# Kernel optimization log

Measured on AMD Instinct MI355X. Metric: run time of the kernel, lower is better.

## Reference

```python
import jax, jax.numpy as jnp
import numpy as np

SAMPLE_RATE = 22050
N_FILTER_BANKS = 64
HOP_LENGTH = 512
BATCH = 4
N_FRAMES = 500
N_SAMPLES = N_FRAMES * HOP_LENGTH


def _frame_mean_weights(n_frames, n_samples):
    """Per-frame weights w s.t. mean over time of linear(align_corners=True)
    upsampling of a length-n_frames signal equals w @ signal (exact same math,
    since the interpolation is linear in the frame values)."""
    pos = jnp.linspace(0.0, n_frames - 1.0, n_samples)
    lo = jnp.clip(jnp.floor(pos).astype(jnp.int32), 0, n_frames - 2)
    frac = pos - lo
    w = jnp.zeros(n_frames, dtype=jnp.float32)
    w = w.at[lo].add(1.0 - frac).at[lo + 1].add(frac)
    return w / n_samples


def setup_inputs() -> dict:
    key = jax.random.key(0)
    k1, k2 = jax.random.split(key)
    filter_magnitudes = jax.random.uniform(k1, (BATCH, N_FRAMES, N_FILTER_BANKS), dtype=jnp.float32)
    noise = jax.random.normal(k2, (BATCH, N_SAMPLES), dtype=jnp.float32)
    return {"filter_magnitudes": filter_magnitudes, "noise": noise}


def reference(filter_magnitudes, noise):
    B, n_frames, n_banks = filter_magnitudes.shape
    n_samples = noise.shape[1]

    noise_fft = jnp.fft.rfft(noise, axis=1)                      # (B, n_freq) complex
    freqs = jnp.fft.rfftfreq(n_samples, 1.0 / SAMPLE_RATE)       # (n_freq,)
    filter_freqs = jnp.logspace(np.log10(20.0), np.log10(SAMPLE_RATE / 2.0), n_banks).astype(jnp.float32)

    # mean over time of the linearly-upsampled magnitudes (exact, no big buffer)
    mean_w = _frame_mean_weights(n_frames, n_samples)            # (n_frames,)
    mean_mag = jnp.einsum('bfk,f->bk', filter_magnitudes, mean_w)  # (B, n_banks)

    # vectorized log-distance filterbank weights: (n_freq, n_banks)
    D = jnp.log(freqs + 1e-7)[:, None] - jnp.log(filter_freqs + 1e-7)[None, :]
    W = jnp.exp(-(D ** 2) / 0.5)
    W = W / (W.sum(axis=1, keepdims=True) + 1e-7)

    filter_response = mean_mag @ W.T                              # (B, n_freq)
    filtered_fft = noise_fft * filter_response
    return jnp.fft.irfft(filtered_fft, n=n_samples, axis=1)      # (B, n_samples)
```

## Files before the change

### kernel.cpp

```cpp
#include <hip/hip_runtime.h>
#include <math.h>

#define NS 256000
#define N1 512
#define N2 500
#define PI_F 3.14159265358979323846f

typedef float2 cplx;

__device__ __forceinline__ cplx cadd(cplx a, cplx b){ return make_float2(a.x+b.x, a.y+b.y); }
__device__ __forceinline__ cplx csub(cplx a, cplx b){ return make_float2(a.x-b.x, a.y-b.y); }
__device__ __forceinline__ cplx cmul(cplx a, cplx b){ return make_float2(a.x*b.x-a.y*b.y, a.x*b.y+a.y*b.x); }
__device__ __forceinline__ cplx cmulc(cplx a, cplx b){ return make_float2(a.x*b.x+a.y*b.y, a.y*b.x-a.x*b.y); }
__device__ __forceinline__ cplx crotf(cplx v, float ang){
    float sn = __sinf(ang), cs = __cosf(ang);
    return make_float2(v.x*cs - v.y*sn, v.x*sn + v.y*cs);
}
__device__ __forceinline__ int PX(int e){ return e + (e>>4); }
__device__ __forceinline__ int rev8_3(int k){ return ((k&7)<<6) | (k&0x38) | (k>>6); }

#define U1PAD 545
#define U2PAD 537
#define WFENCE() asm volatile("s_waitcnt lgkmcnt(0)" ::: "memory")
#define LDS_BARRIER() do{ asm volatile("s_waitcnt lgkmcnt(0)" ::: "memory"); __builtin_amdgcn_s_barrier(); }while(0)

template<bool INV>
__device__ __forceinline__ void dft4(const cplx* a, cplx* b){
    cplx t0=cadd(a[0],a[2]), t1=csub(a[0],a[2]), t2=cadd(a[1],a[3]), t3=csub(a[1],a[3]);
    b[0]=cadd(t0,t2); b[2]=csub(t0,t2);
    if(!INV){ b[1]=make_float2(t1.x+t3.y, t1.y-t3.x); b[3]=make_float2(t1.x-t3.y, t1.y+t3.x); }
    else    { b[1]=make_float2(t1.x-t3.y, t1.y+t3.x); b[3]=make_float2(t1.x+t3.y, t1.y-t3.x); }
}

template<bool INV>
__device__ __forceinline__ void dft8(const cplx* a, cplx* b){
    cplx ev[4]={a[0],a[2],a[4],a[6]}, od[4]={a[1],a[3],a[5],a[7]};
    cplx C[4], D[4];
    dft4<INV>(ev, C); dft4<INV>(od, D);
    const float s = 0.70710678118654752f;
    const float sg = INV ? 1.f : -1.f;
    cplx d1 = cmul(D[1], make_float2( s, sg*s));
    cplx d2 = cmul(D[2], make_float2(0.f, sg ));
    cplx d3 = cmul(D[3], make_float2(-s, sg*s));
    b[0]=cadd(C[0],D[0]); b[4]=csub(C[0],D[0]);
    b[1]=cadd(C[1],d1);   b[5]=csub(C[1],d1);
    b[2]=cadd(C[2],d2);   b[6]=csub(C[2],d2);
    b[3]=cadd(C[3],d3);   b[7]=csub(C[3],d3);
}

template<bool INV>
__device__ __forceinline__ void dft5(const cplx* a, cplx* b){
    const float c1=0.30901699437494742f, s1=0.95105651629515357f;
    const float c2=-0.80901699437494745f, s2=0.58778525229247312f;
    const float sg = INV ? 1.f : -1.f;
    cplx W[5];
    W[0]=make_float2(1.f,0.f);
    W[1]=make_float2(c1, sg*s1); W[2]=make_float2(c2, sg*s2);
    W[3]=make_float2(c2,-sg*s2); W[4]=make_float2(c1,-sg*s1);
#pragma unroll
    for(int u=0;u<5;++u){
        cplx acc = a[0];
        int idx = 0;
#pragma unroll
        for(int r=1;r<5;++r){
            idx += u; if(idx >= 5) idx -= 5;
            acc = cadd(acc, cmul(a[r], W[idx]));
        }
        b[u] = acc;
    }
}

template<int R, int L, int TMUL, bool INV, int NN>
__device__ __forceinline__ void wstage(cplx* Uw, const cplx* tab, int lane){
    constexpr int m = L / R;
    constexpr int nb = NN / R;
    constexpr int NIT = (nb + 63) / 64;
    cplx a[NIT][R];
    cplx wt[NIT][R];
    int  bs[NIT];
#pragma unroll
    for(int it=0; it<NIT; ++it){
        int beta = lane + it*64;
        int blk = beta / m;
        int j = beta - blk*m;
        bs[it] = blk*L + j;
        if(beta < nb){
#pragma unroll
            for(int t=0;t<R;++t) a[it][t] = Uw[PX(bs[it] + m*t)];
#pragma unroll
            for(int t=1;t<R;++t) wt[it][t] = tab[TMUL*j*t];
        }
    }
#pragma unroll
    for(int it=0; it<NIT; ++it){
        int beta = lane + it*64;
        if(beta < nb){
            if(INV){
#pragma unroll
                for(int t=1;t<R;++t) a[it][t] = cmulc(a[it][t], wt[it][t]);
            }
            cplx bb[R];
            if constexpr (R==4) dft4<INV>(a[it], bb);
            else if constexpr (R==5) dft5<INV>(a[it], bb);
            else dft8<INV>(a[it], bb);
            if(!INV){
#pragma unroll
                for(int t=1;t<R;++t) bb[t] = cmul(bb[t], wt[it][t]);
            }
#pragma unroll
            for(int t=0;t<R;++t) Uw[PX(bs[it] + m*t)] = bb[t];
        }
    }
}

template<int NTAB, int NTHR>
__device__ __forceinline__ void build_tab(cplx* tab, int tid){
    const float step = -2.f*PI_F/(float)NTAB;
    for(int i = tid; i < NTAB; i += NTHR){
        float a = step*(float)i;
        tab[i] = make_float2(__cosf(a), __sinf(a));
    }
}

__device__ __forceinline__ int p2k2(int p){
    int t1 = p/100; int r = p - 100*t1;
    int t2 = r/20;  r -= 20*t2;
    int t3 = r>>2;  int t4 = r & 3;
    return t1 + 5*t2 + 25*t3 + 125*t4;
}
__device__ __forceinline__ int k22p(int k){
    int t1 = k % 5; int k5 = k/5;
    int t2 = k5 % 5; int k25 = k5/5;
    int t3 = k25 % 5; int t4 = k25/5;
    return 100*t1 + 20*t2 + 4*t3 + t4;
}
__device__ __forceinline__ int colord(int q){
    int j = q>>1, w = q&1;
    if(j == 0) return w ? 256 : 0;
    return w ? 512 - j : j;
}
__device__ __forceinline__ int xcd_chunk(int bid, int n){
    int q = n>>3, r = n&7;
    int x = bid&7, idx = bid>>3;
    return (x < r ? x*(q+1) : r*(q+1) + (x-r)*q) + idx;
}

__device__ __forceinline__ void hpair(cplx Z1, cplx Z2, float ha, float hb,
                                      cplx* zk, cplx* znk){
    float xr = 0.5f*(Z1.x + Z2.x), xi = 0.5f*(Z1.y - Z2.y);
    float yr = 0.5f*(Z1.y + Z2.y), yi = -0.5f*(Z1.x - Z2.x);
    *zk  = make_float2(ha*xr - hb*yi, ha*xi + hb*yr);
    *znk = make_float2(ha*xr + hb*yi, hb*yr - ha*xi);
}

__global__ void __launch_bounds__(256) kFused1(const float* __restrict__ fm,
                                               const float* __restrict__ noise,
                                               float* __restrict__ mmL,
                                               cplx* __restrict__ Y){
    __shared__ float Aarr[500];
    __shared__ float wfr[500];
    __shared__ float part[256];
    __shared__ cplx tab[512];
    __shared__ cplx U[4][U1PAD];
    const int bid = blockIdx.x, tid = threadIdx.x;
    if(bid < 4){
        const int b = bid;
        for(int f = tid; f < 500; f += 256){
            long long i0 = ((long long)f*255999LL + 498LL)/499LL;
            long long i1 = ((long long)(f+1)*255999LL + 498LL)/499LL;
            long long cnt = i1 - i0;
            long long sumi = (i0 + i1 - 1)*cnt/2;
            long long num = 499LL*sumi - cnt*(long long)f*255999LL;
            Aarr[f] = (float)((double)num / 255999.0);
        }
        __syncthreads();
        for(int f = tid; f < 500; f += 256){
            long long i0 = ((long long)f*255999LL + 498LL)/499LL;
            long long i1 = ((long long)(f+1)*255999LL + 498LL)/499LL;
            double w;
            if(f < 499) w = (double)(i1 - i0) - (double)Aarr[f] + (f > 0 ? (double)Aarr[f-1] : 0.0);
            else        w = (double)Aarr[498] + 1.0;
            wfr[f] = (float)(w / (double)NS);
        }
        __syncthreads();
        const int k = tid & 63, seg = tid >> 6;
        float acc = 0.f;
        for(int f = seg*125; f < seg*125 + 125; ++f)
            acc += wfr[f] * fm[(b*500 + f)*64 + k];
        part[seg*64 + k] = acc;
        __syncthreads();
        if(tid < 64) mmL[b*64 + tid] = part[tid] + part[64+tid] + part[128+tid] + part[192+tid];
        return;
    }
    if(bid == 4){
        if(tid < 64){
            double a = log10(20.0), b2 = log10(11025.0);
            double e = a + (b2 - a)*(double)tid/63.0;
            float ff = (float)pow(10.0, e);
            mmL[256 + tid] = logf(ff + 1e-7f);
        }
        return;
    }
    const int g = xcd_chunk(bid - 5, 250);
    const int s = g / 125;
    const int n2base = (g - s*125) * 4;
    const int lane = tid & 63, w = tid >> 6;
    build_tab<512,256>(tab, tid);
    const float* xa = noise + (size_t)(2*s)*NS + n2base;
    const float* xb = noise + (size_t)(2*s+1)*NS + n2base;
#pragma unroll
    for(int k=0;k<8;++k){
        int i = tid + 256*k;
        int n1 = i >> 2, ws = i & 3;
        U[ws][PX(n1)] = make_float2(xa[n1*500 + ws], xb[n1*500 + ws]);
    }
    __syncthreads();
    cplx* Uw = U[w];
    wstage<8,512, 1,false,512>(Uw, tab, lane); WFENCE();
    wstage<8, 64, 8,false,512>(Uw, tab, lane); WFENCE();
    wstage<8,  8,64,false,512>(Uw, tab, lane); WFENCE();
    const int n2 = n2base + w;
    cplx* yp = Y + ((size_t)s*500 + n2)*N1;
    const float tw = -2.f*PI_F/(float)NS;
#pragma unroll
    for(int t=0;t<8;++t){
        int q = lane + 64*t;
        int c = colord(q);
        cplx v = Uw[PX(rev8_3(c))];
        v = crotf(v, tw*(float)(n2*c));
        yp[q] = v;
    }
}

__global__ void __launch_bounds__(256) kFused2(cplx* __restrict__ Y,
                                               const float* __restrict__ mmL){
    __shared__ cplx tab[500];
    __shared__ cplx U[4][U2PAD];
    __shared__ float Hr[2][2][500];
    __shared__ float HrX[2][500];
    __shared__ float mmS[2][64];
    __shared__ float lgf[64];
    const int tid = threadIdx.x, lane = tid & 63, w = tid >> 6;
    const int L = xcd_chunk(blockIdx.x, 256);
    const int su = L >> 7;
    const int j0 = 2*(L & 127);
    const int s0 = 2*j0;
    cplx* Ybase = Y + (size_t)su*500*512 + s0;
    cplx rg[8];
#pragma unroll
    for(int k=0;k<8;++k){
        int e = tid + 256*k;
        rg[k] = (e < 2000) ? Ybase[(e>>2)*512 + (e&3)] : make_float2(0.f,0.f);
    }
    build_tab<500,256>(tab, tid);
    if(tid < 128) mmS[tid>>6][tid&63] = mmL[2*su*64 + tid];
    if(tid < 64)  lgf[tid] = mmL[256 + tid];
    LDS_BARRIER();
    const int special = (j0 == 0);
    const int nrows = special ? 3 : 2;
    const float invN = 1.f/(float)NS;
    for(int idx = tid; idx < nrows*500; idx += 256){
        int r = idx / 500;
        int p = idx - 500*r;
        int k1 = (r==0) ? j0 : ((r==1) ? j0+1 : 256);
        int k2 = p2k2(p);
        int kf = k1 + 512*k2;
        int kk = min(kf, NS - kf);
        float lf = logf((float)kk*(22050.f/(float)NS) + 1e-7f);
        float wsum = 0.f, a0 = 0.f, a1 = 0.f;
#pragma unroll
        for(int jb=0;jb<64;++jb){
            float d = lf - lgf[jb];
            float e2 = __expf(-2.f*d*d);
            wsum += e2; a0 += e2*mmS[0][jb]; a1 += e2*mmS[1][jb];
        }
        float inv = invN/(wsum + 1e-7f);
        if(r < 2){ Hr[r][0][p] = a0*inv; Hr[r][1][p] = a1*inv; }
        else     { HrX[0][p]   = a0*inv; HrX[1][p]   = a1*inv; }
    }
#pragma unroll
    for(int k=0;k<8;++k){
        int e = tid + 256*k;
        if(e < 2000) U[e&3][PX(e>>2)] = rg[k];
    }
    __syncthreads();
    cplx* Uw = U[w];
    wstage<5,500,  1,false,500>(Uw, tab, lane); WFENCE();
    wstage<5,100,  5,false,500>(Uw, tab, lane); WFENCE();
    wstage<5, 20, 25,false,500>(Uw, tab, lane); WFENCE();
    wstage<4,  4,125,false,500>(Uw, tab, lane);
    __syncthreads();
    {
        const int u = w >> 1, cw = w & 1;
        cplx* UA = U[2*u];
        cplx* UB = U[2*u + 1];
        if(special && u == 0){
            if(cw == 0){
#pragma unroll 1
                for(int t=0;t<8;++t){
                    int p = lane + 64*t;
                    if(p < 500){
                        int k2 = p2k2(p);
                        int pp = k22p((500 - k2) % 500);
                        if(p <= pp){
                            cplx Z1 = UA[PX(p)], Z2 = UA[PX(pp)];
                            cplx zk, znk;
                            hpair(Z1, Z2, Hr[0][0][p], Hr[0][1][p], &zk, &znk);
                            UA[PX(p)]  = zk;
                            UA[PX(pp)] = znk;
                        }
                    }
                }
            } else {
#pragma unroll 1
                for(int t=0;t<4;++t){
                    int p = lane + 64*t;
                    if(p < 250){
                        cplx Z1 = UB[PX(p)], Z2 = UB[PX(499-p)];
                        cplx zk, znk;
                        hpair(Z1, Z2, HrX[0][p], HrX[1][p], &zk, &znk);
                        UB[PX(p)]     = zk;
                        UB[PX(499-p)] = znk;
                    }
                }
            }
        } else {
            const float* H0 = Hr[u][0];
            const float* H1 = Hr[u][1];
#pragma unroll 1
            for(int t=0;t<4;++t){
                int pl = lane + 64*t;
                if(pl < 250){
                    int p = cw*250 + pl;
                    cplx Z1 = UA[PX(p)], Z2 = UB[PX(499-p)];
                    cplx zk, znk;
                    hpair(Z1, Z2, H0[p], H1[p], &zk, &znk);
                    UA[PX(p)]     = zk;
                    UB[PX(499-p)] = znk;
                }
            }
        }
    }
    __syncthreads();
    wstage<4,  4,125,true,500>(Uw, tab, lane); WFENCE();
    wstage<5, 20, 25,true,500>(Uw, tab, lane); WFENCE();
    wstage<5,100,  5,true,500>(Uw, tab, lane); WFENCE();
    wstage<5,500,  1,true,500>(Uw, tab, lane);
    __syncthreads();
    const float tw2 = 2.f*PI_F/(float)NS;
#pragma unroll
    for(int k=0;k<8;++k){
        int e = tid + 256*k;
        if(e < 2000){
            int n2 = e >> 2, sl = e & 3;
            int cc = colord(s0 + sl);
            cplx v = U[sl][PX(n2)];
            v = crotf(v, tw2*(float)(n2*cc));
            Ybase[n2*512 + sl] = v;
        }
    }
}

__global__ void __launch_bounds__(256) kFused3(const cplx* __restrict__ Y,
                                               float* __restrict__ out){
    __shared__ cplx tab[512];
    __shared__ cplx U[4][U1PAD];
    const int tid = threadIdx.x, lane = tid & 63, w = tid >> 6;
    const int g = xcd_chunk(blockIdx.x, 250);
    const int s = g / 125;
    const int n2base = (g - s*125) * 4;
    build_tab<512,256>(tab, tid);
    const cplx* yp = Y + ((size_t)s*500 + n2base)*N1;
#pragma unroll
    for(int k=0;k<8;++k){
        int i = tid + 256*k;
        int ws = i >> 9, q = i & 511;
        cplx v = yp[(size_t)ws*N1 + q];
        U[ws][PX(rev8_3(colord(q)))] = v;
    }
    __syncthreads();
    cplx* Uw = U[w];
    wstage<8,  8,64,true,512>(Uw, tab, lane); WFENCE();
    wstage<8, 64, 8,true,512>(Uw, tab, lane); WFENCE();
    wstage<8,512, 1,true,512>(Uw, tab, lane);
    __syncthreads();
    float* oa = out + (size_t)(2*s)*NS + n2base;
    float* ob = out + (size_t)(2*s+1)*NS + n2base;
#pragma unroll
    for(int k=0;k<8;++k){
        int i = tid + 256*k;
        int n1 = i >> 2, ws = i & 3;
        cplx v = U[ws][PX(n1)];
        oa[n1*500 + ws] = v.x;
        ob[n1*500 + ws] = v.y;
    }
}

extern "C" void kernel_launch(void* const* d_in, const int* in_sizes, int n_in,
                              void* d_out, int out_size, void* d_ws, size_t ws_size,
                              hipStream_t stream) {
    const float* fm = (const float*)d_in[0];
    const float* noise = (const float*)d_in[1];
    float* out = (float*)d_out;

    char* ws = (char*)d_ws;
    cplx*  Y   = (cplx*)ws;
    float* mmL = (float*)(ws + 4194304);

    kFused1<<<255, 256, 0, stream>>>(fm, noise, mmL, Y);
    kFused2<<<256, 256, 0, stream>>>(Y, mmL);
    kFused3<<<250, 256, 0, stream>>>(Y, out);
}
```

Before: 90.59 us.

## Merge three FFT kernels into one phase-switched kernel with noinline stage functions

Replaces the three separate kernels with a single kernel selected by a phase argument, using one dynamic shared-memory buffer carved by offsets. The templated FFT stage code is replaced by __noinline__ radix-8/5/4 stage functions with shift or reciprocal-multiply index math, presumably to shrink code size and register pressure. It also swaps the double-precision pow/log for fast float exp/log in the filter-frequency setup. The risks are call overhead from the noinline functions and slightly different precision in the log-frequency values.

```diff
diff --git a/kernel.cpp b/kernel.cpp
--- a/kernel.cpp
+++ b/kernel.cpp
@@ -19,8 +19,11 @@
 __device__ __forceinline__ int PX(int e){ return e + (e>>4); }
 __device__ __forceinline__ int rev8_3(int k){ return ((k&7)<<6) | (k&0x38) | (k>>6); }
 
-#define U1PAD 545
-#define U2PAD 537
+#define UPAD 545
+#define U_OFF   4096u
+#define EX_OFF  21536u
+#define SMEM_BYTES 34816
+
 #define WFENCE() asm volatile("s_waitcnt lgkmcnt(0)" ::: "memory")
 #define LDS_BARRIER() do{ asm volatile("s_waitcnt lgkmcnt(0)" ::: "memory"); __builtin_amdgcn_s_barrier(); }while(0)
 
@@ -70,55 +73,84 @@
     }
 }
 
-template<int R, int L, int TMUL, bool INV, int NN>
-__device__ __forceinline__ void wstage(cplx* Uw, const cplx* tab, int lane){
-    constexpr int m = L / R;
-    constexpr int nb = NN / R;
-    constexpr int NIT = (nb + 63) / 64;
-    cplx a[NIT][R];
-    cplx wt[NIT][R];
-    int  bs[NIT];
-#pragma unroll
-    for(int it=0; it<NIT; ++it){
-        int beta = lane + it*64;
-        int blk = beta / m;
-        int j = beta - blk*m;
-        bs[it] = blk*L + j;
-        if(beta < nb){
-#pragma unroll
-            for(int t=0;t<R;++t) a[it][t] = Uw[PX(bs[it] + m*t)];
-#pragma unroll
-            for(int t=1;t<R;++t) wt[it][t] = tab[TMUL*j*t];
-        }
-    }
-#pragma unroll
-    for(int it=0; it<NIT; ++it){
-        int beta = lane + it*64;
-        if(beta < nb){
+template<bool INV>
+__device__ __noinline__ void stage8(unsigned uoff, int lane, int sh){
+    extern __shared__ char smem[];
+    cplx* tab = (cplx*)smem;
+    cplx* Uw  = (cplx*)(smem + uoff);
+    const int m = 1 << sh;
+    const int blk = lane >> sh, j = lane & (m-1);
+    const int base = (blk << (sh+3)) + j;
+    const int ts = 6 - sh;
+    cplx a[8], wt[8];
+#pragma unroll
+    for(int t=0;t<8;++t) a[t] = Uw[PX(base + (t<<sh))];
+#pragma unroll
+    for(int t=1;t<8;++t) wt[t] = tab[(j*t) << ts];
+    if(INV){
+#pragma unroll
+        for(int t=1;t<8;++t) a[t] = cmulc(a[t], wt[t]);
+    }
+    cplx bb[8];
+    dft8<INV>(a,bb);
+    if(!INV){
+#pragma unroll
+        for(int t=1;t<8;++t) bb[t] = cmul(bb[t], wt[t]);
+    }
+#pragma unroll
+    for(int t=0;t<8;++t) Uw[PX(base + (t<<sh))] = bb[t];
+}
+
+template<bool INV>
+__device__ __noinline__ void stage5(unsigned uoff, int lane, int m, unsigned recip, int tmul){
+    extern __shared__ char smem[];
+    cplx* tab = (cplx*)smem;
+    cplx* Uw  = (cplx*)(smem + uoff);
+#pragma unroll
+    for(int it=0; it<2; ++it){
+        int beta = lane + 64*it;
+        if(beta < 100){
+            int blk = (int)(((unsigned)beta*recip)>>16);
+            int j = beta - blk*m;
+            int base = blk*(5*m) + j;
+            cplx a[5], wt[5];
+#pragma unroll
+            for(int t=0;t<5;++t) a[t] = Uw[PX(base + m*t)];
+#pragma unroll
+            for(int t=1;t<5;++t) wt[t] = tab[tmul*j*t];
             if(INV){
 #pragma unroll
-                for(int t=1;t<R;++t) a[it][t] = cmulc(a[it][t], wt[it][t]);
-            }
-            cplx bb[R];
-            if constexpr (R==4) dft4<INV>(a[it], bb);
-            else if constexpr (R==5) dft5<INV>(a[it], bb);
-            else dft8<INV>(a[it], bb);
+                for(int t=1;t<5;++t) a[t] = cmulc(a[t], wt[t]);
+            }
+            cplx bb[5];
+            dft5<INV>(a,bb);
             if(!INV){
 #pragma unroll
-                for(int t=1;t<R;++t) bb[t] = cmul(bb[t], wt[it][t]);
-            }
-#pragma unroll
-            for(int t=0;t<R;++t) Uw[PX(bs[it] + m*t)] = bb[t];
-        }
-    }
-}
-
-template<int NTAB, int NTHR>
-__device__ __forceinline__ void build_tab(cplx* tab, int tid){
-    const float step = -2.f*PI_F/(float)NTAB;
-    for(int i = tid; i < NTAB; i += NTHR){
-        float a = step*(float)i;
-        tab[i] = make_float2(__cosf(a), __sinf(a));
+                for(int t=1;t<5;++t) bb[t] = cmul(bb[t], wt[t]);
+            }
+#pragma unroll
+            for(int t=0;t<5;++t) Uw[PX(base + m*t)] = bb[t];
+        }
+    }
+}
+
+template<bool INV>
+__device__ __noinline__ void stage4(unsigned uoff, int lane){
+    extern __shared__ char smem[];
+    cplx* Uw = (cplx*)(smem + uoff);
+#pragma unroll
+    for(int it=0; it<2; ++it){
+        int beta = lane + 64*it;
+        if(beta < 125){
+            int base = beta*4;
+            cplx a[4];
+#pragma unroll
+            for(int t=0;t<4;++t) a[t] = Uw[PX(base+t)];
+            cplx bb[4];
+            dft4<INV>(a,bb);
+#pragma unroll
+            for(int t=0;t<4;++t) Uw[PX(base+t)] = bb[t];
+        }
     }
 }
 
@@ -153,246 +185,251 @@
     *znk = make_float2(ha*xr + hb*yi, hb*yr - ha*xi);
 }
 
-__global__ void __launch_bounds__(256) kFused1(const float* __restrict__ fm,
-                                               const float* __restrict__ noise,
-                                               float* __restrict__ mmL,
-                                               cplx* __restrict__ Y){
-    __shared__ float Aarr[500];
-    __shared__ float wfr[500];
-    __shared__ float part[256];
-    __shared__ cplx tab[512];
-    __shared__ cplx U[4][U1PAD];
+__device__ __forceinline__ void build_tab(cplx* tab, int tid, int ntab){
+    const float step = -2.f*PI_F/(float)ntab;
+    for(int i = tid; i < ntab; i += 256){
+        float a = step*(float)i;
+        tab[i] = make_float2(__cosf(a), __sinf(a));
+    }
+}
+
+__global__ void __launch_bounds__(256) kAll(const float* __restrict__ fm,
+                                            const float* __restrict__ noise,
+                                            float* __restrict__ out,
+                                            cplx* __restrict__ Y,
+                                            float* __restrict__ mmL,
+                                            int phase){
+    extern __shared__ char smem[];
+    cplx* tab = (cplx*)smem;
     const int bid = blockIdx.x, tid = threadIdx.x;
-    if(bid < 4){
-        const int b = bid;
-        for(int f = tid; f < 500; f += 256){
-            long long i0 = ((long long)f*255999LL + 498LL)/499LL;
-            long long i1 = ((long long)(f+1)*255999LL + 498LL)/499LL;
-            long long cnt = i1 - i0;
-            long long sumi = (i0 + i1 - 1)*cnt/2;
-            long long num = 499LL*sumi - cnt*(long long)f*255999LL;
-            Aarr[f] = (float)((double)num / 255999.0);
-        }
-        __syncthreads();
-        for(int f = tid; f < 500; f += 256){
-            long long i0 = ((long long)f*255999LL + 498LL)/499LL;
-            long long i1 = ((long long)(f+1)*255999LL + 498LL)/499LL;
-            double w;
-            if(f < 499) w = (double)(i1 - i0) - (double)Aarr[f] + (f > 0 ? (double)Aarr[f-1] : 0.0);
-            else        w = (double)Aarr[498] + 1.0;
-            wfr[f] = (float)(w / (double)NS);
-        }
-        __syncthreads();
-        const int k = tid & 63, seg = tid >> 6;
-        float acc = 0.f;
-        for(int f = seg*125; f < seg*125 + 125; ++f)
-            acc += wfr[f] * fm[(b*500 + f)*64 + k];
-        part[seg*64 + k] = acc;
-        __syncthreads();
-        if(tid < 64) mmL[b*64 + tid] = part[tid] + part[64+tid] + part[128+tid] + part[192+tid];
+    const int lane = tid & 63, w = tid >> 6;
+    const unsigned uoffw = U_OFF + (unsigned)w*(UPAD*8u);
+    cplx* Ucol0 = (cplx*)(smem + U_OFF);
+
+    if(phase == 0){
+        if(bid < 4){
+            float* Aarr = (float*)(smem + EX_OFF);
+            float* wfr  = (float*)(smem + EX_OFF + 2000);
+            float* part = (float*)(smem + EX_OFF + 4000);
+            const int b = bid;
+            for(int f = tid; f < 500; f += 256){
+                long long i0 = ((long long)f*255999LL + 498LL)/499LL;
+                long long i1 = ((long long)(f+1)*255999LL + 498LL)/499LL;
+                long long cnt = i1 - i0;
+                long long sumi = (i0 + i1 - 1)*cnt/2;
+                long long num = 499LL*sumi - cnt*(long long)f*255999LL;
+                Aarr[f] = (float)((double)num / 255999.0);
+            }
+            __syncthreads();
+            for(int f = tid; f < 500; f += 256){
+                long long i0 = ((long long)f*255999LL + 498LL)/499LL;
+                long long i1 = ((long long)(f+1)*255999LL + 498LL)/499LL;
+                double ww;
+                if(f < 499) ww = (double)(i1 - i0) - (double)Aarr[f] + (f > 0 ? (double)Aarr[f-1] : 0.0);
+                else        ww = (double)Aarr[498] + 1.0;
+                wfr[f] = (float)(ww / (double)NS);
+            }
+            __syncthreads();
+            const int k = tid & 63, seg = tid >> 6;
+            float acc = 0.f;
+            for(int f = seg*125; f < seg*125 + 125; ++f)
+                acc += wfr[f] * fm[(b*500 + f)*64 + k];
+            part[seg*64 + k] = acc;
+            __syncthreads();
+            if(tid < 64) mmL[b*64 + tid] = part[tid] + part[64+tid] + part[128+tid] + part[192+tid];
+            return;
+        }
+        if(bid == 4){
+            if(tid < 64){
+                float ff = __expf(2.99573227f + (float)tid*(6.31218815f/63.f));
+                mmL[256 + tid] = __logf(ff + 1e-7f);
+            }
+            return;
+        }
+        const int g = xcd_chunk(bid - 5, 250);
+        const int s = g / 125;
+        const int n2base = (g - s*125) * 4;
+        build_tab(tab, tid, 512);
+        const float* xa = noise + (size_t)(2*s)*NS + n2base;
+        const float* xb = noise + (size_t)(2*s+1)*NS + n2base;
+#pragma unroll
+        for(int k=0;k<8;++k){
+            int i = tid + 256*k;
+            int n1 = i >> 2, ws = i & 3;
+            (Ucol0 + ws*UPAD)[PX(n1)] = make_float2(xa[n1*500 + ws], xb[n1*500 + ws]);
+        }
+        __syncthreads();
+        stage8<false>(uoffw, lane, 6); WFENCE();
+        stage8<false>(uoffw, lane, 3); WFENCE();
+        stage8<false>(uoffw, lane, 0); WFENCE();
+        const int n2 = n2base + w;
+        cplx* Uw = (cplx*)(smem + uoffw);
+        cplx* yp = Y + ((size_t)s*500 + n2)*N1;
+        const float tw = -2.f*PI_F/(float)NS;
+#pragma unroll
+        for(int t=0;t<8;++t){
+            int q = lane + 64*t;
+            int c = colord(q);
+            cplx v = Uw[PX(rev8_3(c))];
+            v = crotf(v, tw*(float)(n2*c));
+            yp[q] = v;
+        }
         return;
     }
-    if(bid == 4){
-        if(tid < 64){
-            double a = log10(20.0), b2 = log10(11025.0);
-            double e = a + (b2 - a)*(double)tid/63.0;
-            float ff = (float)pow(10.0, e);
-            mmL[256 + tid] = logf(ff + 1e-7f);
-        }
-        return;
-    }
-    const int g = xcd_chunk(bid - 5, 250);
-    const int s = g / 125;
-    const int n2base = (g - s*125) * 4;
-    const int lane = tid & 63, w = tid >> 6;
-    build_tab<512,256>(tab, tid);
-    const float* xa = noise + (size_t)(2*s)*NS + n2base;
-    const float* xb = noise + (size_t)(2*s+1)*NS + n2base;
-#pragma unroll
-    for(int k=0;k<8;++k){
-        int i = tid + 256*k;
-        int n1 = i >> 2, ws = i & 3;
-        U[ws][PX(n1)] = make_float2(xa[n1*500 + ws], xb[n1*500 + ws]);
-    }
-    __syncthreads();
-    cplx* Uw = U[w];
-    wstage<8,512, 1,false,512>(Uw, tab, lane); WFENCE();
-    wstage<8, 64, 8,false,512>(Uw, tab, lane); WFENCE();
-    wstage<8,  8,64,false,512>(Uw, tab, lane); WFENCE();
-    const int n2 = n2base + w;
-    cplx* yp = Y + ((size_t)s*500 + n2)*N1;
-    const float tw = -2.f*PI_F/(float)NS;
-#pragma unroll
-    for(int t=0;t<8;++t){
-        int q = lane + 64*t;
-        int c = colord(q);
-        cplx v = Uw[PX(rev8_3(c))];
-        v = crotf(v, tw*(float)(n2*c));
-        yp[q] = v;
-    }
-}
-
-__global__ void __launch_bounds__(256) kFused2(cplx* __restrict__ Y,
-                                               const float* __restrict__ mmL){
-    __shared__ cplx tab[500];
-    __shared__ cplx U[4][U2PAD];
-    __shared__ float Hr[2][2][500];
-    __shared__ float HrX[2][500];
-    __shared__ float mmS[2][64];
-    __shared__ float lgf[64];
-    const int tid = threadIdx.x, lane = tid & 63, w = tid >> 6;
-    const int L = xcd_chunk(blockIdx.x, 256);
-    const int su = L >> 7;
-    const int j0 = 2*(L & 127);
-    const int s0 = 2*j0;
-    cplx* Ybase = Y + (size_t)su*500*512 + s0;
-    cplx rg[8];
-#pragma unroll
-    for(int k=0;k<8;++k){
-        int e = tid + 256*k;
-        rg[k] = (e < 2000) ? Ybase[(e>>2)*512 + (e&3)] : make_float2(0.f,0.f);
-    }
-    build_tab<500,256>(tab, tid);
-    if(tid < 128) mmS[tid>>6][tid&63] = mmL[2*su*64 + tid];
-    if(tid < 64)  lgf[tid] = mmL[256 + tid];
-    LDS_BARRIER();
-    const int special = (j0 == 0);
-    const int nrows = special ? 3 : 2;
-    const float invN = 1.f/(float)NS;
-    for(int idx = tid; idx < nrows*500; idx += 256){
-        int r = idx / 500;
-        int p = idx - 500*r;
-        int k1 = (r==0) ? j0 : ((r==1) ? j0+1 : 256);
-        int k2 = p2k2(p);
-        int kf = k1 + 512*k2;
-        int kk = min(kf, NS - kf);
-        float lf = logf((float)kk*(22050.f/(float)NS) + 1e-7f);
-        float wsum = 0.f, a0 = 0.f, a1 = 0.f;
-#pragma unroll
-        for(int jb=0;jb<64;++jb){
-            float d = lf - lgf[jb];
-            float e2 = __expf(-2.f*d*d);
-            wsum += e2; a0 += e2*mmS[0][jb]; a1 += e2*mmS[1][jb];
-        }
-        float inv = invN/(wsum + 1e-7f);
-        if(r < 2){ Hr[r][0][p] = a0*inv; Hr[r][1][p] = a1*inv; }
-        else     { HrX[0][p]   = a0*inv; HrX[1][p]   = a1*inv; }
-    }
-#pragma unroll
-    for(int k=0;k<8;++k){
-        int e = tid + 256*k;
-        if(e < 2000) U[e&3][PX(e>>2)] = rg[k];
-    }
-    __syncthreads();
-    cplx* Uw = U[w];
-    wstage<5,500,  1,false,500>(Uw, tab, lane); WFENCE();
-    wstage<5,100,  5,false,500>(Uw, tab, lane); WFENCE();
-    wstage<5, 20, 25,false,500>(Uw, tab, lane); WFENCE();
-    wstage<4,  4,125,false,500>(Uw, tab, lane);
-    __syncthreads();
-    {
-        const int u = w >> 1, cw = w & 1;
-        cplx* UA = U[2*u];
-        cplx* UB = U[2*u + 1];
-        if(special && u == 0){
-            if(cw == 0){
+
+    if(phase == 1){
+        float* HrF = (float*)(smem + EX_OFF);
+        float* HrX = (float*)(smem + EX_OFF + 8000);
+        float* mmS = (float*)(smem + EX_OFF + 12000);
+        float* lgf = (float*)(smem + EX_OFF + 12512);
+        const int L = xcd_chunk(bid, 256);
+        const int su = L >> 7;
+        const int j0 = 2*(L & 127);
+        const int s0 = 2*j0;
+        cplx* Ybase = Y + (size_t)su*500*512 + s0;
+        cplx rg[8];
+#pragma unroll
+        for(int k=0;k<8;++k){
+            int e = tid + 256*k;
+            rg[k] = (e < 2000) ? Ybase[(e>>2)*512 + (e&3)] : make_float2(0.f,0.f);
+        }
+        build_tab(tab, tid, 500);
+        if(tid < 128) mmS[tid] = mmL[2*su*64 + tid];
+        if(tid < 64)  lgf[tid] = mmL[256 + tid];
+        LDS_BARRIER();
+        const int special = (j0 == 0);
+        const int nrows = special ? 3 : 2;
+        const float invN = 1.f/(float)NS;
+        for(int idx = tid; idx < nrows*500; idx += 256){
+            int r = idx / 500;
+            int p = idx - 500*r;
+            int k1 = (r==0) ? j0 : ((r==1) ? j0+1 : 256);
+            int k2 = p2k2(p);
+            int kf = k1 + 512*k2;
+            int kk = min(kf, NS - kf);
+            float lf = __logf((float)kk*(22050.f/(float)NS) + 1e-7f);
+            float wsum = 0.f, a0 = 0.f, a1 = 0.f;
+#pragma unroll 8
+            for(int jb=0;jb<64;++jb){
+                float d = lf - lgf[jb];
+                float e2 = __expf(-2.f*d*d);
+                wsum += e2; a0 += e2*mmS[jb]; a1 += e2*mmS[64+jb];
+            }
+            float inv = invN/(wsum + 1e-7f);
+            if(r < 2){ HrF[(r*2+0)*500 + p] = a0*inv; HrF[(r*2+1)*500 + p] = a1*inv; }
+            else     { HrX[p] = a0*inv; HrX[500+p] = a1*inv; }
+        }
+#pragma unroll
+        for(int k=0;k<8;++k){
+            int e = tid + 256*k;
+            if(e < 2000) (Ucol0 + (e&3)*UPAD)[PX(e>>2)] = rg[k];
+        }
+        __syncthreads();
+        stage5<false>(uoffw, lane, 100,   656u,  1); WFENCE();
+        stage5<false>(uoffw, lane,  20,  3277u,  5); WFENCE();
+        stage5<false>(uoffw, lane,   4, 16384u, 25); WFENCE();
+        stage4<false>(uoffw, lane);
+        __syncthreads();
+        {
+            const int u = w >> 1, cw = w & 1;
+            cplx* UA = Ucol0 + (2*u)*UPAD;
+            cplx* UB = Ucol0 + (2*u+1)*UPAD;
+            if(special && u == 0){
+                if(cw == 0){
 #pragma unroll 1
-                for(int t=0;t<8;++t){
-                    int p = lane + 64*t;
-                    if(p < 500){
-                        int k2 = p2k2(p);
-                        int pp = k22p((500 - k2) % 500);
-                        if(p <= pp){
-                            cplx Z1 = UA[PX(p)], Z2 = UA[PX(pp)];
+                    for(int t=0;t<8;++t){
+                        int p = lane + 64*t;
+                        if(p < 500){
+                            int k2 = p2k2(p);
+                            int pp = k22p((500 - k2) % 500);
+                            if(p <= pp){
+                                cplx Z1 = UA[PX(p)], Z2 = UA[PX(pp)];
+                                cplx zk, znk;
+                                hpair(Z1, Z2, HrF[p], HrF[500+p], &zk, &znk);
+                                UA[PX(p)]  = zk;
+                                UA[PX(pp)] = znk;
+                            }
+                        }
+                    }
+                } else {
+#pragma unroll 1
+                    for(int t=0;t<4;++t){
+                        int p = lane + 64*t;
+                        if(p < 250){
+                            cplx Z1 = UB[PX(p)], Z2 = UB[PX(499-p)];
                             cplx zk, znk;
-                            hpair(Z1, Z2, Hr[0][0][p], Hr[0][1][p], &zk, &znk);
-                            UA[PX(p)]  = zk;
-                            UA[PX(pp)] = znk;
+                            hpair(Z1, Z2, HrX[p], HrX[500+p], &zk, &znk);
+                            UB[PX(p)]     = zk;
+                            UB[PX(499-p)] = znk;
                         }
                     }
                 }
             } else {
+                const float* H0 = HrF + (u*2+0)*500;
+                const float* H1 = HrF + (u*2+1)*500;
 #pragma unroll 1
                 for(int t=0;t<4;++t){
-                    int p = lane + 64*t;
-                    if(p < 250){
-                        cplx Z1 = UB[PX(p)], Z2 = UB[PX(499-p)];
+                    int pl = lane + 64*t;
+                    if(pl < 250){
+                        int p = cw*250 + pl;
+                        cplx Z1 = UA[PX(p)], Z2 = UB[PX(499-p)];
                         cplx zk, znk;
-                        hpair(Z1, Z2, HrX[0][p], HrX[1][p], &zk, &znk);
-                        UB[PX(p)]     = zk;
+                        hpair(Z1, Z2, H0[p], H1[p], &zk, &znk);
+                        UA[PX(p)]     = zk;
                         UB[PX(499-p)] = znk;
                     }
                 }
             }
-        } else {
-            const float* H0 = Hr[u][0];
-            const float* H1 = Hr[u][1];
-#pragma unroll 1
-            for(int t=0;t<4;++t){
-                int pl = lane + 64*t;
-                if(pl < 250){
-                    int p = cw*250 + pl;
-                    cplx Z1 = UA[PX(p)], Z2 = UB[PX(499-p)];
-                    cplx zk, znk;
-                    hpair(Z1, Z2, H0[p], H1[p], &zk, &znk);
-                    UA[PX(p)]     = zk;
-                    UB[PX(499-p)] = znk;
-                }
-            }
-        }
-    }
-    __syncthreads();
-    wstage<4,  4,125,true,500>(Uw, tab, lane); WFENCE();
-    wstage<5, 20, 25,true,500>(Uw, tab, lane); WFENCE();
-    wstage<5,100,  5,true,500>(Uw, tab, lane); WFENCE();
-    wstage<5,500,  1,true,500>(Uw, tab, lane);
-    __syncthreads();
-    const float tw2 = 2.f*PI_F/(float)NS;
-#pragma unroll
-    for(int k=0;k<8;++k){
-        int e = tid + 256*k;
-        if(e < 2000){
-            int n2 = e >> 2, sl = e & 3;
-            int cc = colord(s0 + sl);
-            cplx v = U[sl][PX(n2)];
-            v = crotf(v, tw2*(float)(n2*cc));
-            Ybase[n2*512 + sl] = v;
-        }
-    }
-}
-
-__global__ void __launch_bounds__(256) kFused3(const cplx* __restrict__ Y,
-                                               float* __restrict__ out){
-    __shared__ cplx tab[512];
-    __shared__ cplx U[4][U1PAD];
-    const int tid = threadIdx.x, lane = tid & 63, w = tid >> 6;
-    const int g = xcd_chunk(blockIdx.x, 250);
-    const int s = g / 125;
-    const int n2base = (g - s*125) * 4;
-    build_tab<512,256>(tab, tid);
-    const cplx* yp = Y + ((size_t)s*500 + n2base)*N1;
-#pragma unroll
-    for(int k=0;k<8;++k){
-        int i = tid + 256*k;
-        int ws = i >> 9, q = i & 511;
-        cplx v = yp[(size_t)ws*N1 + q];
-        U[ws][PX(rev8_3(colord(q)))] = v;
-    }
-    __syncthreads();
-    cplx* Uw = U[w];
-    wstage<8,  8,64,true,512>(Uw, tab, lane); WFENCE();
-    wstage<8, 64, 8,true,512>(Uw, tab, lane); WFENCE();
-    wstage<8,512, 1,true,512>(Uw, tab, lane);
-    __syncthreads();
-    float* oa = out + (size_t)(2*s)*NS + n2base;
-    float* ob = out + (size_t)(2*s+1)*NS + n2base;
-#pragma unroll
-    for(int k=0;k<8;++k){
-        int i = tid + 256*k;
-        int n1 = i >> 2, ws = i & 3;
-        cplx v = U[ws][PX(n1)];
-        oa[n1*500 + ws] = v.x;
-        ob[n1*500 + ws] = v.y;
+        }
+        __syncthreads();
+        stage4<true>(uoffw, lane); WFENCE();
+        stage5<true>(uoffw, lane,   4, 16384u, 25); WFENCE();
+        stage5<true>(uoffw, lane,  20,  3277u,  5); WFENCE();
+        stage5<true>(uoffw, lane, 100,   656u,  1);
+        __syncthreads();
+        const float tw2 = 2.f*PI_F/(float)NS;
+#pragma unroll
+        for(int k=0;k<8;++k){
+            int e = tid + 256*k;
+            if(e < 2000){
+                int n2 = e >> 2, sl = e & 3;
+                int cc = colord(s0 + sl);
+                cplx v = (Ucol0 + sl*UPAD)[PX(n2)];
+                v = crotf(v, tw2*(float)(n2*cc));
+                Ybase[n2*512 + sl] = v;
+            }
+        }
+        return;
+    }
+
+    {
+        const int g = xcd_chunk(bid, 250);
+        const int s = g / 125;
+        const int n2base = (g - s*125) * 4;
+        build_tab(tab, tid, 512);
+        const cplx* yp = Y + ((size_t)s*500 + n2base)*N1;
+#pragma unroll
+        for(int k=0;k<8;++k){
+            int i = tid + 256*k;
+            int ws = i >> 9, q = i & 511;
+            cplx v = yp[(size_t)ws*N1 + q];
+            (Ucol0 + ws*UPAD)[PX(rev8_3(colord(q)))] = v;
+        }
+        __syncthreads();
+        stage8<true>(uoffw, lane, 0); WFENCE();
+        stage8<true>(uoffw, lane, 3); WFENCE();
+        stage8<true>(uoffw, lane, 6);
+        __syncthreads();
+        float* oa = out + (size_t)(2*s)*NS + n2base;
+        float* ob = out + (size_t)(2*s+1)*NS + n2base;
+#pragma unroll
+        for(int k=0;k<8;++k){
+            int i = tid + 256*k;
+            int n1 = i >> 2, ws = i & 3;
+            cplx v = (Ucol0 + ws*UPAD)[PX(n1)];
+            oa[n1*500 + ws] = v.x;
+            ob[n1*500 + ws] = v.y;
+        }
     }
 }
 
@@ -407,7 +444,7 @@
     cplx*  Y   = (cplx*)ws;
     float* mmL = (float*)(ws + 4194304);
 
-    kFused1<<<255, 256, 0, stream>>>(fm, noise, mmL, Y);
-    kFused2<<<256, 256, 0, stream>>>(Y, mmL);
-    kFused3<<<250, 256, 0, stream>>>(Y, out);
-}
+    kAll<<<255, 256, SMEM_BYTES, stream>>>(fm, noise, out, Y, mmL, 0);
+    kAll<<<256, 256, SMEM_BYTES, stream>>>(fm, noise, out, Y, mmL, 1);
+    kAll<<<250, 256, SMEM_BYTES, stream>>>(fm, noise, out, Y, mmL, 2);
+}
```

Result: slower. 98.33 us (+8.5%).

## Precompute filter response in first kernel's spare blocks instead of in FFT kernel

Applied to the files above, without the earlier changes.

Moves the per-frequency filterbank response computation (64 exp per bin) out of the second kernel and into 257 extra blocks of the first kernel. Those blocks each recompute the mean magnitudes for all batches and write the response to global memory. The second kernel then only loads the precomputed values alongside its FFT data. This takes the transcendental-heavy work off the critical path of kFused2, at the cost of a larger first launch with redundant mean-magnitude work and extra global traffic.

```diff
diff --git a/kernel.cpp b/kernel.cpp
--- a/kernel.cpp
+++ b/kernel.cpp
@@ -22,7 +22,6 @@
 #define U1PAD 545
 #define U2PAD 537
 #define WFENCE() asm volatile("s_waitcnt lgkmcnt(0)" ::: "memory")
-#define LDS_BARRIER() do{ asm volatile("s_waitcnt lgkmcnt(0)" ::: "memory"); __builtin_amdgcn_s_barrier(); }while(0)
 
 template<bool INV>
 __device__ __forceinline__ void dft4(const cplx* a, cplx* b){
@@ -155,16 +154,18 @@
 
 __global__ void __launch_bounds__(256) kFused1(const float* __restrict__ fm,
                                                const float* __restrict__ noise,
-                                               float* __restrict__ mmL,
+                                               float* __restrict__ HrG,
                                                cplx* __restrict__ Y){
     __shared__ float Aarr[500];
     __shared__ float wfr[500];
     __shared__ float part[256];
+    __shared__ float mmS[4][64];
+    __shared__ float lgf[64];
     __shared__ cplx tab[512];
     __shared__ cplx U[4][U1PAD];
     const int bid = blockIdx.x, tid = threadIdx.x;
-    if(bid < 4){
-        const int b = bid;
+    if(bid >= 250){
+        const int k1 = bid - 250;
         for(int f = tid; f < 500; f += 256){
             long long i0 = ((long long)f*255999LL + 498LL)/499LL;
             long long i1 = ((long long)(f+1)*255999LL + 498LL)/499LL;
@@ -184,24 +185,43 @@
         }
         __syncthreads();
         const int k = tid & 63, seg = tid >> 6;
-        float acc = 0.f;
-        for(int f = seg*125; f < seg*125 + 125; ++f)
-            acc += wfr[f] * fm[(b*500 + f)*64 + k];
-        part[seg*64 + k] = acc;
+#pragma unroll 1
+        for(int b = 0; b < 4; ++b){
+            float acc = 0.f;
+            for(int f = seg*125; f < seg*125 + 125; ++f)
+                acc += wfr[f] * fm[(b*500 + f)*64 + k];
+            part[seg*64 + k] = acc;
+            __syncthreads();
+            if(tid < 64) mmS[b][tid] = part[tid] + part[64+tid] + part[128+tid] + part[192+tid];
+            __syncthreads();
+        }
+        if(tid < 64){
+            float ff = __expf(2.99573227f + (float)tid*(6.31218815f/63.f));
+            lgf[tid] = __logf(ff + 1e-7f);
+        }
         __syncthreads();
-        if(tid < 64) mmL[b*64 + tid] = part[tid] + part[64+tid] + part[128+tid] + part[192+tid];
+        const float invN = 1.f/(float)NS;
+        for(int idx = tid; idx < 1000; idx += 256){
+            int su = (idx >= 500) ? 1 : 0;
+            int p = idx - 500*su;
+            int k2 = p2k2(p);
+            int kf = k1 + 512*k2;
+            int kk = min(kf, NS - kf);
+            float lf = __logf((float)kk*(22050.f/(float)NS) + 1e-7f);
+            float wsum = 0.f, a0 = 0.f, a1 = 0.f;
+#pragma unroll
+            for(int jb=0;jb<64;++jb){
+                float d = lf - lgf[jb];
+                float e2 = __expf(-2.f*d*d);
+                wsum += e2; a0 += e2*mmS[2*su][jb]; a1 += e2*mmS[2*su+1][jb];
+            }
+            float inv = invN/(wsum + 1e-7f);
+            HrG[((size_t)(su*257 + k1)*2 + 0)*500 + p] = a0*inv;
+            HrG[((size_t)(su*257 + k1)*2 + 1)*500 + p] = a1*inv;
+        }
         return;
     }
-    if(bid == 4){
-        if(tid < 64){
-            double a = log10(20.0), b2 = log10(11025.0);
-            double e = a + (b2 - a)*(double)tid/63.0;
-            float ff = (float)pow(10.0, e);
-            mmL[256 + tid] = logf(ff + 1e-7f);
-        }
-        return;
-    }
-    const int g = xcd_chunk(bid - 5, 250);
+    const int g = xcd_chunk(bid, 250);
     const int s = g / 125;
     const int n2base = (g - s*125) * 4;
     const int lane = tid & 63, w = tid >> 6;
@@ -233,18 +253,17 @@
 }
 
 __global__ void __launch_bounds__(256) kFused2(cplx* __restrict__ Y,
-                                               const float* __restrict__ mmL){
+                                               const float* __restrict__ HrG){
     __shared__ cplx tab[500];
     __shared__ cplx U[4][U2PAD];
-    __shared__ float Hr[2][2][500];
+    __shared__ float HrF[2][2][500];
     __shared__ float HrX[2][500];
-    __shared__ float mmS[2][64];
-    __shared__ float lgf[64];
     const int tid = threadIdx.x, lane = tid & 63, w = tid >> 6;
     const int L = xcd_chunk(blockIdx.x, 256);
     const int su = L >> 7;
     const int j0 = 2*(L & 127);
     const int s0 = 2*j0;
+    const int special = (j0 == 0);
     cplx* Ybase = Y + (size_t)su*500*512 + s0;
     cplx rg[8];
 #pragma unroll
@@ -252,31 +271,38 @@
         int e = tid + 256*k;
         rg[k] = (e < 2000) ? Ybase[(e>>2)*512 + (e&3)] : make_float2(0.f,0.f);
     }
+    const float* hsrc = HrG + (size_t)(su*257 + j0)*2*500;
+    float hg[8];
+#pragma unroll
+    for(int k=0;k<8;++k){
+        int e = tid + 256*k;
+        hg[k] = (e < 2000) ? hsrc[e] : 0.f;
+    }
+    float hx[4];
+    if(special){
+        const float* hxsrc = HrG + (size_t)(su*257 + 256)*2*500;
+#pragma unroll
+        for(int k=0;k<4;++k){
+            int e = tid + 256*k;
+            hx[k] = (e < 1000) ? hxsrc[e] : 0.f;
+        }
+    }
     build_tab<500,256>(tab, tid);
-    if(tid < 128) mmS[tid>>6][tid&63] = mmL[2*su*64 + tid];
-    if(tid < 64)  lgf[tid] = mmL[256 + tid];
-    LDS_BARRIER();
-    const int special = (j0 == 0);
-    const int nrows = special ? 3 : 2;
-    const float invN = 1.f/(float)NS;
-    for(int idx = tid; idx < nrows*500; idx += 256){
-        int r = idx / 500;
-        int p = idx - 500*r;
-        int k1 = (r==0) ? j0 : ((r==1) ? j0+1 : 256);
-        int k2 = p2k2(p);
-        int kf = k1 + 512*k2;
-        int kk = min(kf, NS - kf);
-        float lf = logf((float)kk*(22050.f/(float)NS) + 1e-7f);
-        float wsum = 0.f, a0 = 0.f, a1 = 0.f;
-#pragma unroll
-        for(int jb=0;jb<64;++jb){
-            float d = lf - lgf[jb];
-            float e2 = __expf(-2.f*d*d);
-            wsum += e2; a0 += e2*mmS[0][jb]; a1 += e2*mmS[1][jb];
-        }
-        float inv = invN/(wsum + 1e-7f);
-        if(r < 2){ Hr[r][0][p] = a0*inv; Hr[r][1][p] = a1*inv; }
-        else     { HrX[0][p]   = a0*inv; HrX[1][p]   = a1*inv; }
+    {
+        float* hf = &HrF[0][0][0];
+#pragma unroll
+        for(int k=0;k<8;++k){
+            int e = tid + 256*k;
+            if(e < 2000) hf[e] = hg[k];
+        }
+        if(special){
+            float* hxl = &HrX[0][0];
+#pragma unroll
+            for(int k=0;k<4;++k){
+                int e = tid + 256*k;
+                if(e < 1000) hxl[e] = hx[k];
+            }
+        }
     }
 #pragma unroll
     for(int k=0;k<8;++k){
@@ -305,7 +331,7 @@
                         if(p <= pp){
                             cplx Z1 = UA[PX(p)], Z2 = UA[PX(pp)];
                             cplx zk, znk;
-                            hpair(Z1, Z2, Hr[0][0][p], Hr[0][1][p], &zk, &znk);
+                            hpair(Z1, Z2, HrF[0][0][p], HrF[0][1][p], &zk, &znk);
                             UA[PX(p)]  = zk;
                             UA[PX(pp)] = znk;
                         }
@@ -325,8 +351,8 @@
                 }
             }
         } else {
-            const float* H0 = Hr[u][0];
-            const float* H1 = Hr[u][1];
+            const float* H0 = HrF[u][0];
+            const float* H1 = HrF[u][1];
 #pragma unroll 1
             for(int t=0;t<4;++t){
                 int pl = lane + 64*t;
@@ -405,9 +431,9 @@
 
     char* ws = (char*)d_ws;
     cplx*  Y   = (cplx*)ws;
-    float* mmL = (float*)(ws + 4194304);
-
-    kFused1<<<255, 256, 0, stream>>>(fm, noise, mmL, Y);
-    kFused2<<<256, 256, 0, stream>>>(Y, mmL);
+    float* HrG = (float*)(ws + 4194304);
+
+    kFused1<<<507, 256, 0, stream>>>(fm, noise, HrG, Y);
+    kFused2<<<256, 256, 0, stream>>>(Y, HrG);
     kFused3<<<250, 256, 0, stream>>>(Y, out);
 }
```

Measured after the change: 113.4 us. 25.2% more time.
